# Kernel optimization log

Measured on AMD Instinct MI355X. Metric: run time of the kernel, lower is better.

The kernel has to match this reference:

```python
import jax, jax.numpy as jnp
import numpy as np
import math

# dims
B, S, HID = 1, 4096, 2048
NH = 16            # num_attention_heads
Q_LORA = 768
KV_LORA = 512
D_ROPE = 64        # qk_rope_head_dim
D_V = 128          # v_head_dim
TOP_K = 1024       # dsa_top_k
EPS = 1e-6
ROPE_BASE = 1e7
YARN_SCALE = 32.0


def _rms_norm(x, w, eps=EPS):
    xf = x.astype(jnp.float32)
    var = jnp.mean(xf * xf, axis=-1, keepdims=True)
    return (w * (xf * jax.lax.rsqrt(var + eps))).astype(x.dtype)


def _rotate_half(x):
    h = x.shape[-1] // 2
    return jnp.concatenate([-x[..., h:], x[..., :h]], axis=-1)


def _yarn_cos_sin(seq_len):
    # _yarn_find_correction_dims returns (mid, mid) => entire inv_freq is interpolated (divided by scale)
    inv_freq = 1.0 / (ROPE_BASE ** (jnp.arange(0, D_ROPE, 2, dtype=jnp.float32) / D_ROPE))
    inv_freq = inv_freq / YARN_SCALE
    t = jnp.arange(seq_len, dtype=jnp.float32) / YARN_SCALE
    freqs = t[:, None] * inv_freq[None, :]          # [S, D_ROPE/2]
    emb = jnp.concatenate([freqs, freqs], axis=-1)  # [S, D_ROPE]
    mscale2 = (0.1 * math.log(YARN_SCALE) + 1.0) ** 2  # mscale * mscale_all_dim
    return jnp.cos(emb) * mscale2, jnp.sin(emb) * mscale2


def setup_inputs() -> dict:
    key = jax.random.key(0)
    ks = jax.random.split(key, 10)
    std = 0.02
    return {
        'hidden_states': jax.random.normal(ks[0], (B, S, HID), dtype=jnp.float32),
        'position_ids': jnp.broadcast_to(jnp.arange(S), (B, S)),
        'dsa_indices': jnp.sort(jax.random.randint(ks[1], (B, 1, TOP_K), 0, S), axis=-1),
        'wq_a': jax.random.normal(ks[2], (HID, Q_LORA), dtype=jnp.float32) * std,
        'q_a_ln_w': jnp.ones((Q_LORA,), dtype=jnp.float32),
        'wq_b': jax.random.normal(ks[3], (Q_LORA, NH * D_V), dtype=jnp.float32) * std,
        'wq_rope': jax.random.normal(ks[4], (Q_LORA, NH * D_ROPE), dtype=jnp.float32) * std,
        'wkv_a': jax.random.normal(ks[5], (HID, KV_LORA + D_ROPE), dtype=jnp.float32) * std,
        'kv_a_ln_w': jnp.ones((KV_LORA,), dtype=jnp.float32),
        'wkv_b': jax.random.normal(ks[6], (KV_LORA, NH * 2 * D_V), dtype=jnp.float32) * std,
        'wo': jax.random.normal(ks[7], (NH * D_V, HID), dtype=jnp.float32) * std,
    }


def reference(hidden_states, position_ids, dsa_indices, wq_a, q_a_ln_w, wq_b,
              wq_rope, wkv_a, kv_a_ln_w, wkv_b, wo):
    bsz, seq_len, _ = hidden_states.shape

    # low-rank Q path (MLA)
    q_latent = _rms_norm(hidden_states @ wq_a, q_a_ln_w)            # [B,S,Q_LORA]
    q = (q_latent @ wq_b).reshape(bsz, seq_len, NH, D_V)            # [B,S,H,D_V]
    q_rope = (q_latent @ wq_rope).reshape(bsz, seq_len, NH, D_ROPE)

    # low-rank KV path with MQA rope channel
    kv_lr = hidden_states @ wkv_a                                   # [B,S,KV_LORA+D_ROPE]
    kv_latent = _rms_norm(kv_lr[..., :KV_LORA], kv_a_ln_w)
    k_rope = kv_lr[..., KV_LORA:]                                   # [B,S,D_ROPE]
    k_and_v = (kv_latent @ wkv_b).reshape(bsz, seq_len, NH, 2 * D_V)
    k = k_and_v[..., :D_V]
    v = k_and_v[..., D_V:]
    k_rope = jnp.broadcast_to(k_rope[:, :, None, :], (bsz, seq_len, NH, D_ROPE))

    # YaRN rotary embedding
    cos, sin = _yarn_cos_sin(seq_len)                               # [S,D_ROPE]
    cos_p = cos[position_ids][:, :, None, :]                        # [B,S,1,D_ROPE]
    sin_p = sin[position_ids][:, :, None, :]
    q_rope = q_rope * cos_p + _rotate_half(q_rope) * sin_p
    k_rope = k_rope * cos_p + _rotate_half(k_rope) * sin_p

    q_full = jnp.concatenate([q, q_rope], axis=-1)                  # [B,S,H,D_V+D_ROPE]
    k_full = jnp.concatenate([k, k_rope], axis=-1)

    # DSA: gather top-k KV positions per batch (dsa_indices[b,0,:])
    idx = dsa_indices[:, 0, :]                                      # [B,TOP_K]
    k_g = jnp.take_along_axis(k_full, idx[:, :, None, None], axis=1)  # [B,K,H,D]
    v_g = jnp.take_along_axis(v, idx[:, :, None, None], axis=1)       # [B,K,H,D_V]

    scale = 1.0 / math.sqrt(D_V + D_ROPE)
    scores = jnp.einsum('bqhd,bkhd->bhqk', q_full, k_g) * scale     # [B,H,S,K]
    probs = jax.nn.softmax(scores, axis=-1)
    attn = jnp.einsum('bhqk,bkhd->bqhd', probs, v_g)                # [B,S,H,D_V]
    out = attn.reshape(bsz, seq_len, NH * D_V) @ wo                 # [B,S,HID]
    return out
```

## Files before the change

kernel.cpp:

```cpp
#include <hip/hip_runtime.h>
#include <hip/hip_bf16.h>
#include <math.h>

#define S_LEN 4096
#define HIDDEN 2048
#define NH 16
#define QLORA 768
#define KVLORA 512
#define DROPE 64
#define DV 128
#define TOPK 1024
#define DQK 192

typedef __attribute__((ext_vector_type(4))) float f32x4;
typedef __attribute__((ext_vector_type(8))) __bf16 bf16x8;
typedef __attribute__((ext_vector_type(8))) unsigned short ushort8;
typedef unsigned short u16;
typedef unsigned int u32;

__device__ __forceinline__ u16 f2bf(float f) {
    union { float f; u32 u; } v; v.f = f;
    u32 r = v.u + 0x7fffu + ((v.u >> 16) & 1u);
    return (u16)(r >> 16);
}

__global__ __launch_bounds__(256) void k_cast(const float* __restrict__ src,
                                              u16* __restrict__ dst, int n4) {
    int i = blockIdx.x * 256 + threadIdx.x;
    if (i >= n4) return;
    float4 v = ((const float4*)src)[i];
    union { u16 h[4]; uint2 u; } o;
    o.h[0] = f2bf(v.x); o.h[1] = f2bf(v.y);
    o.h[2] = f2bf(v.z); o.h[3] = f2bf(v.w);
    ((uint2*)dst)[i] = o.u;
}

__global__ __launch_bounds__(256) void k_yarn(const int* __restrict__ pos_ids,
                                              float* __restrict__ cos_t,
                                              float* __restrict__ sin_t) {
    int idx = blockIdx.x * 256 + threadIdx.x;
    if (idx >= S_LEN * 32) return;
    int s = idx >> 5, i = idx & 31;
    float pos = (float)pos_ids[s];
    float inv = expf(-(float)i * 0.503690489092448f) * (1.0f / 1024.0f);
    float ang = pos * inv;
    const float MS2 = 1.8132604f;
    float sv, cv;
    sincosf(ang, &sv, &cv);
    cos_t[idx] = cv * MS2;
    sin_t[idx] = sv * MS2;
}

__global__ __launch_bounds__(256) void k_transpose(const float* __restrict__ src,
                                                   u16* __restrict__ dst,
                                                   int K, int N) {
    __shared__ u16 t[32][33];
    int n0 = blockIdx.x * 32, k0 = blockIdx.y * 32;
    int tx = threadIdx.x & 31, ty = threadIdx.x >> 5;
    #pragma unroll
    for (int i = 0; i < 32; i += 8)
        t[ty + i][tx] = f2bf(src[(long)(k0 + ty + i) * N + n0 + tx]);
    __syncthreads();
    #pragma unroll
    for (int i = 0; i < 32; i += 8)
        dst[(long)(n0 + ty + i) * K + k0 + tx] = t[tx][ty + i];
}

template <int MODE>
__global__ __launch_bounds__(256) void k_gemm(const u16* __restrict__ A,
                                              const u16* __restrict__ Bt,
                                              void* __restrict__ out0,
                                              void* __restrict__ out1,
                                              int M, int N, int K) {
    __shared__ u16 lA[128 * 40];
    __shared__ u16 lB[128 * 40];
    const int bm = blockIdx.y, bn = blockIdx.x;
    const int tid = threadIdx.x;
    const int lane = tid & 63, wid = tid >> 6;
    const int wr = wid >> 1, wc = wid & 1;
    const int l15 = lane & 15, l4 = lane >> 4;

    f32x4 acc[4][4];
    #pragma unroll
    for (int i = 0; i < 4; ++i)
        #pragma unroll
        for (int j = 0; j < 4; ++j) acc[i][j] = f32x4{0.f, 0.f, 0.f, 0.f};

    const int r = tid >> 1;
    const int ko = (tid & 1) * 16;
    const long arow = (long)bm * 128 + r;
    const int bcol = bn * 128 + r;
    const u16* pA = A + arow * K + ko;
    const u16* pB = Bt + (long)bcol * K + ko;
    const bool bok = (bcol < N);

    const int nkt = K >> 5;
    for (int kt = 0; kt < nkt; ++kt) {
        uint4 a0 = *(const uint4*)(pA);
        uint4 a1 = *(const uint4*)(pA + 8);
        uint4 b0 = bok ? *(const uint4*)(pB) : uint4{0, 0, 0, 0};
        uint4 b1 = bok ? *(const uint4*)(pB + 8) : uint4{0, 0, 0, 0};
        pA += 32; pB += 32;
        *(uint4*)(&lA[r * 40 + ko]) = a0;
        *(uint4*)(&lA[r * 40 + ko + 8]) = a1;
        *(uint4*)(&lB[r * 40 + ko]) = b0;
        *(uint4*)(&lB[r * 40 + ko + 8]) = b1;
        __syncthreads();

        bf16x8 af[4], bfr[4];
        #pragma unroll
        for (int mr = 0; mr < 4; ++mr)
            af[mr] = *(const bf16x8*)(&lA[(wr * 64 + mr * 16 + l15) * 40 + l4 * 8]);
        #pragma unroll
        for (int nc = 0; nc < 4; ++nc)
            bfr[nc] = *(const bf16x8*)(&lB[(wc * 64 + nc * 16 + l15) * 40 + l4 * 8]);
        #pragma unroll
        for (int mr = 0; mr < 4; ++mr)
            #pragma unroll
            for (int nc = 0; nc < 4; ++nc)
                acc[mr][nc] = __builtin_amdgcn_mfma_f32_16x16x32_bf16(
                    af[mr], bfr[nc], acc[mr][nc], 0, 0, 0);
        __syncthreads();
    }

    const int row0 = bm * 128 + wr * 64;
    const int col0 = bn * 128 + wc * 64;
    #pragma unroll
    for (int mr = 0; mr < 4; ++mr) {
        #pragma unroll
        for (int nc = 0; nc < 4; ++nc) {
            #pragma unroll
            for (int jj = 0; jj < 4; ++jj) {
                int row = row0 + mr * 16 + l4 * 4 + jj;
                int col = col0 + nc * 16 + l15;
                if (col >= N) continue;
                float v = acc[mr][nc][jj];
                if (MODE == 0) {
                    if (col < QLORA)
                        ((float*)out0)[(long)row * QLORA + col] = v;
                    else
                        ((float*)out1)[(long)row * (KVLORA + DROPE) + (col - QLORA)] = v;
                } else if (MODE == 1) {
                    if (col < NH * DV) {
                        int h = col >> 7, d = col & 127;
                        ((u16*)out0)[((long)h * S_LEN + row) * DQK + d] = f2bf(v);
                    } else {
                        int c2 = col - NH * DV;
                        ((u16*)out1)[(long)row * (NH * DROPE) + c2] = f2bf(v);
                    }
                } else if (MODE == 2) {
                    int h = col >> 8, rr = col & 255;
                    if (rr < 128)
                        ((u16*)out0)[((long)h * S_LEN + row) * DV + rr] = f2bf(v);
                    else
                        ((u16*)out1)[((long)h * S_LEN + row) * DV + (rr - 128)] = f2bf(v);
                } else {
                    ((float*)out0)[(long)row * N + col] = v;
                }
            }
        }
    }
}

__global__ __launch_bounds__(256) void k_rms_q(const float* __restrict__ q_lr,
                                               const float* __restrict__ w,
                                               u16* __restrict__ q_latent) {
    int s = blockIdx.x;
    const float* x = q_lr + (long)s * QLORA;
    int t = threadIdx.x;
    float v0 = x[t], v1 = x[t + 256], v2 = x[t + 512];
    float ss = v0 * v0 + v1 * v1 + v2 * v2;
    #pragma unroll
    for (int off = 32; off >= 1; off >>= 1) ss += __shfl_xor(ss, off);
    __shared__ float red[4];
    if ((t & 63) == 0) red[t >> 6] = ss;
    __syncthreads();
    ss = red[0] + red[1] + red[2] + red[3];
    float inv = rsqrtf(ss / (float)QLORA + 1e-6f);
    u16* o = q_latent + (long)s * QLORA;
    o[t]       = f2bf(v0 * inv * w[t]);
    o[t + 256] = f2bf(v1 * inv * w[t + 256]);
    o[t + 512] = f2bf(v2 * inv * w[t + 512]);
}

__global__ __launch_bounds__(256) void k_kv_norm_rope(const float* __restrict__ kv_lr,
                                                      const float* __restrict__ w,
                                                      const float* __restrict__ cos_t,
                                                      const float* __restrict__ sin_t,
                                                      u16* __restrict__ kv_latent,
                                                      u16* __restrict__ krope) {
    int s = blockIdx.x;
    const float* x = kv_lr + (long)s * (KVLORA + DROPE);
    int t = threadIdx.x;
    float v0 = x[t], v1 = x[t + 256];
    float ss = v0 * v0 + v1 * v1;
    #pragma unroll
    for (int off = 32; off >= 1; off >>= 1) ss += __shfl_xor(ss, off);
    __shared__ float red[4];
    if ((t & 63) == 0) red[t >> 6] = ss;
    __syncthreads();
    ss = red[0] + red[1] + red[2] + red[3];
    float inv = rsqrtf(ss / (float)KVLORA + 1e-6f);
    u16* o = kv_latent + (long)s * KVLORA;
    o[t]       = f2bf(v0 * inv * w[t]);
    o[t + 256] = f2bf(v1 * inv * w[t + 256]);
    if (t < DROPE) {
        int i = t & 31;
        float c = cos_t[s * 32 + i], sn = sin_t[s * 32 + i];
        float xr = x[KVLORA + t];
        float xp = x[KVLORA + ((t < 32) ? t + 32 : t - 32)];
        float val = (t < 32) ? xr * c - xp * sn : xr * c + xp * sn;
        krope[(long)s * DROPE + t] = f2bf(val);
    }
}

__global__ __launch_bounds__(256) void k_rope_q(const u16* __restrict__ q_rope_raw,
                                                const float* __restrict__ cos_t,
                                                const float* __restrict__ sin_t,
                                                u16* __restrict__ q_full) {
    long idx = (long)blockIdx.x * 256 + threadIdx.x;
    int s = (int)(idx >> 10);
    int rem = (int)(idx & 1023);
    int h = rem >> 6, j = rem & 63;
    int i = j & 31;
    float c = cos_t[s * 32 + i], sn = sin_t[s * 32 + i];
    const u16* base = q_rope_raw + (long)s * (NH * DROPE) + h * DROPE;
    union { u32 u; float f; } xr, xp;
    xr.u = ((u32)base[j]) << 16;
    xp.u = ((u32)base[(j < 32) ? j + 32 : j - 32]) << 16;
    float val = (j < 32) ? xr.f * c - xp.f * sn : xr.f * c + xp.f * sn;
    q_full[((long)h * S_LEN + s) * DQK + DV + j] = f2bf(val);
}

__global__ void k_gather(const int* __restrict__ idx,
                         const u16* __restrict__ k_buf,
                         const u16* __restrict__ v_buf,
                         const u16* __restrict__ krope,
                         u16* __restrict__ k_g, u16* __restrict__ v_g) {
    int j = blockIdx.x, h = blockIdx.y, t = threadIdx.x;
    int src = idx[j];
    const uint4* kb = (const uint4*)(k_buf + ((long)h * S_LEN + src) * DV);
    const uint4* vb = (const uint4*)(v_buf + ((long)h * S_LEN + src) * DV);
    const uint4* kr = (const uint4*)(krope + (long)src * DROPE);
    uint4* kgp = (uint4*)(k_g + ((long)h * TOPK + j) * DQK);
    uint4* vgp = (uint4*)(v_g + ((long)h * TOPK + j) * DV);
    if (t < 16)       kgp[t] = kb[t];
    else if (t < 24)  kgp[t] = kr[t - 16];
    else if (t < 40)  vgp[t - 24] = vb[t - 24];
}

__global__ __launch_bounds__(256) void k_attn(const u16* __restrict__ qf,
                                              const u16* __restrict__ kg,
                                              const u16* __restrict__ vg,
                                              u16* __restrict__ attn_out) {
    __shared__ u16 lK[64 * 200];
    __shared__ u16 lV[128 * 72];
    __shared__ u16 lP[4 * 16 * 72];
    const int h = blockIdx.y, qt = blockIdx.x;
    const int tid = threadIdx.x, lane = tid & 63, wid = tid >> 6;
    const int l15 = lane & 15, l4 = lane >> 4;

    bf16x8 qfr[6];
    {
        const u16* qrow = qf + ((long)h * S_LEN + qt * 64 + wid * 16 + l15) * DQK + l4 * 8;
        #pragma unroll
        for (int kd = 0; kd < 6; ++kd) qfr[kd] = *(const bf16x8*)(qrow + kd * 32);
    }
    float m[4] = {-1e30f, -1e30f, -1e30f, -1e30f};
    float l[4] = {0.f, 0.f, 0.f, 0.f};
    f32x4 acc_o[8];
    #pragma unroll
    for (int nc = 0; nc < 8; ++nc) acc_o[nc] = f32x4{0.f, 0.f, 0.f, 0.f};

    const int krow = tid >> 2, kseg = (tid & 3) * 48;
    const int vkey = tid >> 2, vseg = (tid & 3) * 32;
    const float scale = 0.07216878364870323f;

    for (int kt = 0; kt < TOPK / 64; ++kt) {
        {
            const u16* src = kg + ((long)h * TOPK + kt * 64 + krow) * DQK + kseg;
            u16* dst = &lK[krow * 200 + kseg];
            #pragma unroll
            for (int u = 0; u < 6; ++u)
                *(uint4*)(dst + u * 8) = *(const uint4*)(src + u * 8);
        }
        {
            const u16* src = vg + ((long)h * TOPK + kt * 64 + vkey) * DV + vseg;
            ushort8 dv[4];
            #pragma unroll
            for (int u = 0; u < 4; ++u) dv[u] = *(const ushort8*)(src + u * 8);
            #pragma unroll
            for (int u = 0; u < 4; ++u)
                #pragma unroll
                for (int e = 0; e < 8; ++e)
                    lV[(vseg + u * 8 + e) * 72 + vkey] = dv[u][e];
        }
        __syncthreads();

        f32x4 sa[4];
        #pragma unroll
        for (int kc = 0; kc < 4; ++kc) {
            sa[kc] = f32x4{0.f, 0.f, 0.f, 0.f};
            #pragma unroll
            for (int kd = 0; kd < 6; ++kd) {
                bf16x8 kf = *(const bf16x8*)(&lK[(kc * 16 + l15) * 200 + kd * 32 + l4 * 8]);
                sa[kc] = __builtin_amdgcn_mfma_f32_16x16x32_bf16(qfr[kd], kf, sa[kc], 0, 0, 0);
            }
            sa[kc] *= scale;
        }
        float fac[4], psum[4];
        #pragma unroll
        for (int jj = 0; jj < 4; ++jj) {
            float mx = fmaxf(fmaxf(sa[0][jj], sa[1][jj]), fmaxf(sa[2][jj], sa[3][jj]));
            #pragma unroll
            for (int off = 1; off <= 8; off <<= 1) mx = fmaxf(mx, __shfl_xor(mx, off));
            float mnew = fmaxf(m[jj], mx);
            fac[jj] = __expf(m[jj] - mnew);
            m[jj] = mnew;
            psum[jj] = 0.f;
        }
        #pragma unroll
        for (int kc = 0; kc < 4; ++kc) {
            #pragma unroll
            for (int jj = 0; jj < 4; ++jj) {
                float p = __expf(sa[kc][jj] - m[jj]);
                psum[jj] += p;
                lP[(wid * 16 + l4 * 4 + jj) * 72 + kc * 16 + l15] = f2bf(p);
            }
        }
        #pragma unroll
        for (int jj = 0; jj < 4; ++jj) {
            #pragma unroll
            for (int off = 1; off <= 8; off <<= 1) psum[jj] += __shfl_xor(psum[jj], off);
            l[jj] = l[jj] * fac[jj] + psum[jj];
        }
        #pragma unroll
        for (int nc = 0; nc < 8; ++nc)
            #pragma unroll
            for (int jj = 0; jj < 4; ++jj) acc_o[nc][jj] *= fac[jj];
        #pragma unroll
        for (int kc2 = 0; kc2 < 2; ++kc2) {
            bf16x8 pf = *(const bf16x8*)(&lP[(wid * 16 + l15) * 72 + kc2 * 32 + l4 * 8]);
            #pragma unroll
            for (int nc = 0; nc < 8; ++nc) {
                bf16x8 vf = *(const bf16x8*)(&lV[(nc * 16 + l15) * 72 + kc2 * 32 + l4 * 8]);
                acc_o[nc] = __builtin_amdgcn_mfma_f32_16x16x32_bf16(pf, vf, acc_o[nc], 0, 0, 0);
            }
        }
        __syncthreads();
    }
    int row = qt * 64 + wid * 16 + l4 * 4;
    #pragma unroll
    for (int nc = 0; nc < 8; ++nc)
        #pragma unroll
        for (int jj = 0; jj < 4; ++jj) {
            float v = acc_o[nc][jj] / l[jj];
            attn_out[(long)(row + jj) * (NH * DV) + h * DV + nc * 16 + l15] = f2bf(v);
        }
}

extern "C" void kernel_launch(void* const* d_in, const int* in_sizes, int n_in,
                              void* d_out, int out_size, void* d_ws, size_t ws_size,
                              hipStream_t stream) {
    const float* hs      = (const float*)d_in[0];
    const int*   pos     = (const int*)d_in[1];
    const int*   dsa     = (const int*)d_in[2];
    const float* wq_a    = (const float*)d_in[3];
    const float* q_ln    = (const float*)d_in[4];
    const float* wq_b    = (const float*)d_in[5];
    const float* wq_rope = (const float*)d_in[6];
    const float* wkv_a   = (const float*)d_in[7];
    const float* kv_ln   = (const float*)d_in[8];
    const float* wkv_b   = (const float*)d_in[9];
    const float* wo      = (const float*)d_in[10];
    float* out = (float*)d_out;

    char* ws = (char*)d_ws;
    auto alloc = [&](size_t bytes) {
        char* p = ws; ws += (bytes + 255) & ~(size_t)255; return p;
    };
    u16* W1t  = (u16*)alloc(1344L * 2048 * 2);
    u16* W2t  = (u16*)alloc(3072L * 768 * 2);
    u16* W3t  = (u16*)alloc(4096L * 512 * 2);
    u16* W4t  = (u16*)alloc(2048L * 2048 * 2);
    float* q_lr  = (float*)alloc(4096L * 768 * 4);
    float* kv_lr = (float*)alloc(4096L * 576 * 4);
    u16* q_latent   = (u16*)alloc(4096L * 768 * 2);
    u16* kv_latent  = (u16*)alloc(4096L * 512 * 2);
    u16* q_rope_raw = (u16*)alloc(4096L * 1024 * 2);
    u16* q_full     = (u16*)alloc(16L * 4096 * 192 * 2);
    u16* k_buf      = (u16*)alloc(16L * 4096 * 128 * 2);
    u16* v_buf      = (u16*)alloc(16L * 4096 * 128 * 2);
    float* cos_t    = (float*)alloc(4096L * 32 * 4);
    float* sin_t    = (float*)alloc(4096L * 32 * 4);
    char* late = alloc(16L * 4096 * 2 * 2 > (16L * 1024 * 192 + 16L * 1024 * 128 + 4096L * 64) * 2
                       ? 16L * 4096 * 2 * 2
                       : (16L * 1024 * 192 + 16L * 1024 * 128 + 4096L * 64) * 2);
    u16* hs_bf = (u16*)late;
    u16* k_g   = (u16*)late;
    u16* v_g   = k_g + 16L * 1024 * 192;
    u16* krope = v_g + 16L * 1024 * 128;
    u16* attn_o = (u16*)q_lr;

    k_yarn<<<dim3(512), dim3(256), 0, stream>>>(pos, cos_t, sin_t);
    k_cast<<<dim3(8192), dim3(256), 0, stream>>>(hs, hs_bf, 4096 * 2048 / 4);

    k_transpose<<<dim3(768 / 32, 2048 / 32), 256, 0, stream>>>(wq_a, W1t, 2048, 768);
    k_transpose<<<dim3(576 / 32, 2048 / 32), 256, 0, stream>>>(wkv_a, W1t + 768L * 2048, 2048, 576);
    k_transpose<<<dim3(2048 / 32, 768 / 32), 256, 0, stream>>>(wq_b, W2t, 768, 2048);
    k_transpose<<<dim3(1024 / 32, 768 / 32), 256, 0, stream>>>(wq_rope, W2t + 2048L * 768, 768, 1024);
    k_transpose<<<dim3(4096 / 32, 512 / 32), 256, 0, stream>>>(wkv_b, W3t, 512, 4096);
    k_transpose<<<dim3(2048 / 32, 2048 / 32), 256, 0, stream>>>(wo, W4t, 2048, 2048);

    k_gemm<0><<<dim3(11, 32), 256, 0, stream>>>(hs_bf, W1t, q_lr, kv_lr, 4096, 1344, 2048);
    k_rms_q<<<4096, 256, 0, stream>>>(q_lr, q_ln, q_latent);
    k_kv_norm_rope<<<4096, 256, 0, stream>>>(kv_lr, kv_ln, cos_t, sin_t, kv_latent, krope);
    k_gemm<1><<<dim3(24, 32), 256, 0, stream>>>(q_latent, W2t, q_full, q_rope_raw, 4096, 3072, 768);
    k_rope_q<<<16384, 256, 0, stream>>>(q_rope_raw, cos_t, sin_t, q_full);
    k_gemm<2><<<dim3(32, 32), 256, 0, stream>>>(kv_latent, W3t, k_buf, v_buf, 4096, 4096, 512);
    k_gather<<<dim3(1024, 16), 64, 0, stream>>>(dsa, k_buf, v_buf, krope, k_g, v_g);
    k_attn<<<dim3(64, 16), 256, 0, stream>>>(q_full, k_g, v_g, attn_o);
    k_gemm<3><<<dim3(16, 32), 256, 0, stream>>>(attn_o, W4t, out, nullptr, 4096, 2048, 2048);
}
```

Baseline: 513.7 us.

## Use direct global-to-LDS loads in GEMM, fuse q RoPE, pre-transpose V, widen attention tiles

The GEMM now stages A and B tiles with global_load_lds (16-byte async copies straight into unpadded LDS) instead of register round-trips, and pads W1t to 1408 columns so the N bound check can go. Query RoPE is fused into the MODE 1 GEMM epilogue, which removes the separate rope kernel and the q_rope_raw buffer. The gather kernel writes V pre-transposed per 64-key tile so attention can copy it into LDS with vector stores, and attention now handles 128 queries per block with a remapped head/tile order. Risks: the unpadded LDS may cause bank conflicts, the padded W1t rows are never written (their outputs are discarded), and the attention block holds more registers.

Result: faster. 502.4 us (-2.2%).

```diff
diff --git a/kernel.cpp b/kernel.cpp
--- a/kernel.cpp
+++ b/kernel.cpp
@@ -14,7 +14,6 @@
 
 typedef __attribute__((ext_vector_type(4))) float f32x4;
 typedef __attribute__((ext_vector_type(8))) __bf16 bf16x8;
-typedef __attribute__((ext_vector_type(8))) unsigned short ushort8;
 typedef unsigned short u16;
 typedef unsigned int u32;
 
@@ -22,6 +21,10 @@
     union { float f; u32 u; } v; v.f = f;
     u32 r = v.u + 0x7fffu + ((v.u >> 16) & 1u);
     return (u16)(r >> 16);
+}
+
+__device__ __forceinline__ void gll16(const u16* g, u16* l) {
+    __builtin_amdgcn_global_load_lds((const void*)g, (void*)l, 16, 0, 0);
 }
 
 __global__ __launch_bounds__(256) void k_cast(const float* __restrict__ src,
@@ -71,9 +74,11 @@
                                               const u16* __restrict__ Bt,
                                               void* __restrict__ out0,
                                               void* __restrict__ out1,
+                                              const float* __restrict__ cos_t,
+                                              const float* __restrict__ sin_t,
                                               int M, int N, int K) {
-    __shared__ u16 lA[128 * 40];
-    __shared__ u16 lB[128 * 40];
+    __shared__ u16 lA[128 * 32];
+    __shared__ u16 lB[128 * 32];
     const int bm = blockIdx.y, bn = blockIdx.x;
     const int tid = threadIdx.x;
     const int lane = tid & 63, wid = tid >> 6;
@@ -86,34 +91,31 @@
         #pragma unroll
         for (int j = 0; j < 4; ++j) acc[i][j] = f32x4{0.f, 0.f, 0.f, 0.f};
 
-    const int r = tid >> 1;
-    const int ko = (tid & 1) * 16;
-    const long arow = (long)bm * 128 + r;
-    const int bcol = bn * 128 + r;
-    const u16* pA = A + arow * K + ko;
-    const u16* pB = Bt + (long)bcol * K + ko;
-    const bool bok = (bcol < N);
+    const int srow = wid * 32 + (lane >> 2);
+    const int scol = (lane & 3) * 8;
+    const u16* gA = A + (long)(bm * 128 + srow) * K + scol;
+    const u16* gB = Bt + (long)(bn * 128 + srow) * K + scol;
+    u16* lA0 = lA + wid * 1024;
+    u16* lB0 = lB + wid * 1024;
+    const long kstep16 = 16L * K;
 
     const int nkt = K >> 5;
     for (int kt = 0; kt < nkt; ++kt) {
-        uint4 a0 = *(const uint4*)(pA);
-        uint4 a1 = *(const uint4*)(pA + 8);
-        uint4 b0 = bok ? *(const uint4*)(pB) : uint4{0, 0, 0, 0};
-        uint4 b1 = bok ? *(const uint4*)(pB + 8) : uint4{0, 0, 0, 0};
-        pA += 32; pB += 32;
-        *(uint4*)(&lA[r * 40 + ko]) = a0;
-        *(uint4*)(&lA[r * 40 + ko + 8]) = a1;
-        *(uint4*)(&lB[r * 40 + ko]) = b0;
-        *(uint4*)(&lB[r * 40 + ko + 8]) = b1;
+        const u16* pa = gA + kt * 32;
+        const u16* pb = gB + kt * 32;
+        gll16(pa, lA0);
+        gll16(pa + kstep16, lA0 + 512);
+        gll16(pb, lB0);
+        gll16(pb + kstep16, lB0 + 512);
         __syncthreads();
 
         bf16x8 af[4], bfr[4];
         #pragma unroll
         for (int mr = 0; mr < 4; ++mr)
-            af[mr] = *(const bf16x8*)(&lA[(wr * 64 + mr * 16 + l15) * 40 + l4 * 8]);
+            af[mr] = *(const bf16x8*)(&lA[(wr * 64 + mr * 16 + l15) * 32 + l4 * 8]);
         #pragma unroll
         for (int nc = 0; nc < 4; ++nc)
-            bfr[nc] = *(const bf16x8*)(&lB[(wc * 64 + nc * 16 + l15) * 40 + l4 * 8]);
+            bfr[nc] = *(const bf16x8*)(&lB[(wc * 64 + nc * 16 + l15) * 32 + l4 * 8]);
         #pragma unroll
         for (int mr = 0; mr < 4; ++mr)
             #pragma unroll
@@ -133,12 +135,11 @@
             for (int jj = 0; jj < 4; ++jj) {
                 int row = row0 + mr * 16 + l4 * 4 + jj;
                 int col = col0 + nc * 16 + l15;
-                if (col >= N) continue;
                 float v = acc[mr][nc][jj];
                 if (MODE == 0) {
                     if (col < QLORA)
                         ((float*)out0)[(long)row * QLORA + col] = v;
-                    else
+                    else if (col < QLORA + KVLORA + DROPE)
                         ((float*)out1)[(long)row * (KVLORA + DROPE) + (col - QLORA)] = v;
                 } else if (MODE == 1) {
                     if (col < NH * DV) {
@@ -146,7 +147,11 @@
                         ((u16*)out0)[((long)h * S_LEN + row) * DQK + d] = f2bf(v);
                     } else {
                         int c2 = col - NH * DV;
-                        ((u16*)out1)[(long)row * (NH * DROPE) + c2] = f2bf(v);
+                        int h = c2 >> 6, j = c2 & 63, i = j & 31;
+                        float c = cos_t[row * 32 + i], sn = sin_t[row * 32 + i];
+                        float xp = acc[mr][nc ^ 2][jj];
+                        float val = (j < 32) ? v * c - xp * sn : v * c + xp * sn;
+                        ((u16*)out0)[((long)h * S_LEN + row) * DQK + DV + j] = f2bf(val);
                     }
                 } else if (MODE == 2) {
                     int h = col >> 8, rr = col & 255;
@@ -214,66 +219,58 @@
     }
 }
 
-__global__ __launch_bounds__(256) void k_rope_q(const u16* __restrict__ q_rope_raw,
-                                                const float* __restrict__ cos_t,
-                                                const float* __restrict__ sin_t,
-                                                u16* __restrict__ q_full) {
-    long idx = (long)blockIdx.x * 256 + threadIdx.x;
-    int s = (int)(idx >> 10);
-    int rem = (int)(idx & 1023);
-    int h = rem >> 6, j = rem & 63;
-    int i = j & 31;
-    float c = cos_t[s * 32 + i], sn = sin_t[s * 32 + i];
-    const u16* base = q_rope_raw + (long)s * (NH * DROPE) + h * DROPE;
-    union { u32 u; float f; } xr, xp;
-    xr.u = ((u32)base[j]) << 16;
-    xp.u = ((u32)base[(j < 32) ? j + 32 : j - 32]) << 16;
-    float val = (j < 32) ? xr.f * c - xp.f * sn : xr.f * c + xp.f * sn;
-    q_full[((long)h * S_LEN + s) * DQK + DV + j] = f2bf(val);
-}
-
 __global__ void k_gather(const int* __restrict__ idx,
                          const u16* __restrict__ k_buf,
                          const u16* __restrict__ v_buf,
                          const u16* __restrict__ krope,
-                         u16* __restrict__ k_g, u16* __restrict__ v_g) {
+                         u16* __restrict__ k_g, u16* __restrict__ v_g_t) {
     int j = blockIdx.x, h = blockIdx.y, t = threadIdx.x;
     int src = idx[j];
     const uint4* kb = (const uint4*)(k_buf + ((long)h * S_LEN + src) * DV);
-    const uint4* vb = (const uint4*)(v_buf + ((long)h * S_LEN + src) * DV);
     const uint4* kr = (const uint4*)(krope + (long)src * DROPE);
     uint4* kgp = (uint4*)(k_g + ((long)h * TOPK + j) * DQK);
-    uint4* vgp = (uint4*)(v_g + ((long)h * TOPK + j) * DV);
     if (t < 16)       kgp[t] = kb[t];
     else if (t < 24)  kgp[t] = kr[t - 16];
-    else if (t < 40)  vgp[t - 24] = vb[t - 24];
+    u32 vv = *(const u32*)(v_buf + ((long)h * S_LEN + src) * DV + t * 2);
+    int kt = j >> 6, jin = j & 63;
+    u16* base = v_g_t + ((long)(h * 16 + kt) * 128) * 64 + jin;
+    base[(2 * t) * 64]     = (u16)(vv & 0xffff);
+    base[(2 * t + 1) * 64] = (u16)(vv >> 16);
 }
 
 __global__ __launch_bounds__(256) void k_attn(const u16* __restrict__ qf,
                                               const u16* __restrict__ kg,
-                                              const u16* __restrict__ vg,
+                                              const u16* __restrict__ vgt,
                                               u16* __restrict__ attn_out) {
     __shared__ u16 lK[64 * 200];
-    __shared__ u16 lV[128 * 72];
-    __shared__ u16 lP[4 * 16 * 72];
-    const int h = blockIdx.y, qt = blockIdx.x;
+    __shared__ u16 lVt[128 * 72];
+    __shared__ u16 lP[4][16 * 72];
+    const int b = blockIdx.x;
+    const int h = (b & 7) * 2 + ((b >> 3) & 1);
+    const int qt = b >> 4;
     const int tid = threadIdx.x, lane = tid & 63, wid = tid >> 6;
     const int l15 = lane & 15, l4 = lane >> 4;
 
-    bf16x8 qfr[6];
-    {
-        const u16* qrow = qf + ((long)h * S_LEN + qt * 64 + wid * 16 + l15) * DQK + l4 * 8;
-        #pragma unroll
-        for (int kd = 0; kd < 6; ++kd) qfr[kd] = *(const bf16x8*)(qrow + kd * 32);
-    }
-    float m[4] = {-1e30f, -1e30f, -1e30f, -1e30f};
-    float l[4] = {0.f, 0.f, 0.f, 0.f};
-    f32x4 acc_o[8];
-    #pragma unroll
-    for (int nc = 0; nc < 8; ++nc) acc_o[nc] = f32x4{0.f, 0.f, 0.f, 0.f};
+    bf16x8 qfr[2][6];
+    #pragma unroll
+    for (int qs = 0; qs < 2; ++qs) {
+        const u16* qrow = qf + ((long)h * S_LEN + qt * 128 + wid * 32 + qs * 16 + l15) * DQK + l4 * 8;
+        #pragma unroll
+        for (int kd = 0; kd < 6; ++kd) qfr[qs][kd] = *(const bf16x8*)(qrow + kd * 32);
+    }
+    float m[2][4], l[2][4];
+    #pragma unroll
+    for (int qs = 0; qs < 2; ++qs)
+        #pragma unroll
+        for (int jj = 0; jj < 4; ++jj) { m[qs][jj] = -1e30f; l[qs][jj] = 0.f; }
+    f32x4 acc_o[2][8];
+    #pragma unroll
+    for (int qs = 0; qs < 2; ++qs)
+        #pragma unroll
+        for (int nc = 0; nc < 8; ++nc) acc_o[qs][nc] = f32x4{0.f, 0.f, 0.f, 0.f};
 
     const int krow = tid >> 2, kseg = (tid & 3) * 48;
-    const int vkey = tid >> 2, vseg = (tid & 3) * 32;
+    u16* lPw = lP[wid];
     const float scale = 0.07216878364870323f;
 
     for (int kt = 0; kt < TOPK / 64; ++kt) {
@@ -285,78 +282,80 @@
                 *(uint4*)(dst + u * 8) = *(const uint4*)(src + u * 8);
         }
         {
-            const u16* src = vg + ((long)h * TOPK + kt * 64 + vkey) * DV + vseg;
-            ushort8 dv[4];
-            #pragma unroll
-            for (int u = 0; u < 4; ++u) dv[u] = *(const ushort8*)(src + u * 8);
-            #pragma unroll
-            for (int u = 0; u < 4; ++u)
-                #pragma unroll
-                for (int e = 0; e < 8; ++e)
-                    lV[(vseg + u * 8 + e) * 72 + vkey] = dv[u][e];
+            const u16* src = vgt + ((long)(h * 16 + kt) * 128) * 64 + tid * 32;
+            u16* dst = &lVt[(tid >> 1) * 72 + (tid & 1) * 32];
+            #pragma unroll
+            for (int c = 0; c < 4; ++c)
+                *(uint4*)(dst + c * 8) = *(const uint4*)(src + c * 8);
         }
         __syncthreads();
 
-        f32x4 sa[4];
-        #pragma unroll
-        for (int kc = 0; kc < 4; ++kc) {
-            sa[kc] = f32x4{0.f, 0.f, 0.f, 0.f};
-            #pragma unroll
-            for (int kd = 0; kd < 6; ++kd) {
-                bf16x8 kf = *(const bf16x8*)(&lK[(kc * 16 + l15) * 200 + kd * 32 + l4 * 8]);
-                sa[kc] = __builtin_amdgcn_mfma_f32_16x16x32_bf16(qfr[kd], kf, sa[kc], 0, 0, 0);
-            }
-            sa[kc] *= scale;
-        }
-        float fac[4], psum[4];
-        #pragma unroll
-        for (int jj = 0; jj < 4; ++jj) {
-            float mx = fmaxf(fmaxf(sa[0][jj], sa[1][jj]), fmaxf(sa[2][jj], sa[3][jj]));
-            #pragma unroll
-            for (int off = 1; off <= 8; off <<= 1) mx = fmaxf(mx, __shfl_xor(mx, off));
-            float mnew = fmaxf(m[jj], mx);
-            fac[jj] = __expf(m[jj] - mnew);
-            m[jj] = mnew;
-            psum[jj] = 0.f;
-        }
-        #pragma unroll
-        for (int kc = 0; kc < 4; ++kc) {
+        #pragma unroll
+        for (int qs = 0; qs < 2; ++qs) {
+            f32x4 sa[4];
+            #pragma unroll
+            for (int kc = 0; kc < 4; ++kc) {
+                sa[kc] = f32x4{0.f, 0.f, 0.f, 0.f};
+                #pragma unroll
+                for (int kd = 0; kd < 6; ++kd) {
+                    bf16x8 kf = *(const bf16x8*)(&lK[(kc * 16 + l15) * 200 + kd * 32 + l4 * 8]);
+                    sa[kc] = __builtin_amdgcn_mfma_f32_16x16x32_bf16(qfr[qs][kd], kf, sa[kc], 0, 0, 0);
+                }
+                sa[kc] *= scale;
+            }
+            float fac[4], psum[4];
             #pragma unroll
             for (int jj = 0; jj < 4; ++jj) {
-                float p = __expf(sa[kc][jj] - m[jj]);
-                psum[jj] += p;
-                lP[(wid * 16 + l4 * 4 + jj) * 72 + kc * 16 + l15] = f2bf(p);
-            }
-        }
-        #pragma unroll
-        for (int jj = 0; jj < 4; ++jj) {
-            #pragma unroll
-            for (int off = 1; off <= 8; off <<= 1) psum[jj] += __shfl_xor(psum[jj], off);
-            l[jj] = l[jj] * fac[jj] + psum[jj];
-        }
-        #pragma unroll
-        for (int nc = 0; nc < 8; ++nc)
-            #pragma unroll
-            for (int jj = 0; jj < 4; ++jj) acc_o[nc][jj] *= fac[jj];
-        #pragma unroll
-        for (int kc2 = 0; kc2 < 2; ++kc2) {
-            bf16x8 pf = *(const bf16x8*)(&lP[(wid * 16 + l15) * 72 + kc2 * 32 + l4 * 8]);
-            #pragma unroll
-            for (int nc = 0; nc < 8; ++nc) {
-                bf16x8 vf = *(const bf16x8*)(&lV[(nc * 16 + l15) * 72 + kc2 * 32 + l4 * 8]);
-                acc_o[nc] = __builtin_amdgcn_mfma_f32_16x16x32_bf16(pf, vf, acc_o[nc], 0, 0, 0);
+                float mx = fmaxf(fmaxf(sa[0][jj], sa[1][jj]), fmaxf(sa[2][jj], sa[3][jj]));
+                #pragma unroll
+                for (int off = 1; off <= 8; off <<= 1) mx = fmaxf(mx, __shfl_xor(mx, off));
+                float mnew = fmaxf(m[qs][jj], mx);
+                fac[jj] = __expf(m[qs][jj] - mnew);
+                m[qs][jj] = mnew;
+                psum[jj] = 0.f;
+            }
+            #pragma unroll
+            for (int kc = 0; kc < 4; ++kc) {
+                #pragma unroll
+                for (int jj = 0; jj < 4; ++jj) {
+                    float p = __expf(sa[kc][jj] - m[qs][jj]);
+                    psum[jj] += p;
+                    lPw[(l4 * 4 + jj) * 72 + kc * 16 + l15] = f2bf(p);
+                }
+            }
+            #pragma unroll
+            for (int jj = 0; jj < 4; ++jj) {
+                #pragma unroll
+                for (int off = 1; off <= 8; off <<= 1) psum[jj] += __shfl_xor(psum[jj], off);
+                l[qs][jj] = l[qs][jj] * fac[jj] + psum[jj];
+            }
+            #pragma unroll
+            for (int nc = 0; nc < 8; ++nc)
+                #pragma unroll
+                for (int jj = 0; jj < 4; ++jj) acc_o[qs][nc][jj] *= fac[jj];
+            #pragma unroll
+            for (int kc2 = 0; kc2 < 2; ++kc2) {
+                bf16x8 pf = *(const bf16x8*)(&lPw[l15 * 72 + kc2 * 32 + l4 * 8]);
+                #pragma unroll
+                for (int nc = 0; nc < 8; ++nc) {
+                    bf16x8 vf = *(const bf16x8*)(&lVt[(nc * 16 + l15) * 72 + kc2 * 32 + l4 * 8]);
+                    acc_o[qs][nc] = __builtin_amdgcn_mfma_f32_16x16x32_bf16(pf, vf, acc_o[qs][nc], 0, 0, 0);
+                }
             }
         }
         __syncthreads();
     }
-    int row = qt * 64 + wid * 16 + l4 * 4;
-    #pragma unroll
-    for (int nc = 0; nc < 8; ++nc)
-        #pragma unroll
-        for (int jj = 0; jj < 4; ++jj) {
-            float v = acc_o[nc][jj] / l[jj];
-            attn_out[(long)(row + jj) * (NH * DV) + h * DV + nc * 16 + l15] = f2bf(v);
-        }
+    #pragma unroll
+    for (int qs = 0; qs < 2; ++qs) {
+        int row = qt * 128 + wid * 32 + qs * 16 + l4 * 4;
+        #pragma unroll
+        for (int nc = 0; nc < 8; ++nc)
+            #pragma unroll
+            for (int jj = 0; jj < 4; ++jj) {
+                float v = acc_o[qs][nc][jj] / l[qs][jj];
+                attn_out[(long)(row + jj) * (NH * DV) + h * DV + nc * 16 + l15] = f2bf(v);
+            }
+    }
 }
 
 extern "C" void kernel_launch(void* const* d_in, const int* in_sizes, int n_in,
@@ -379,7 +378,7 @@
     auto alloc = [&](size_t bytes) {
         char* p = ws; ws += (bytes + 255) & ~(size_t)255; return p;
     };
-    u16* W1t  = (u16*)alloc(1344L * 2048 * 2);
+    u16* W1t  = (u16*)alloc(1408L * 2048 * 2);
     u16* W2t  = (u16*)alloc(3072L * 768 * 2);
     u16* W3t  = (u16*)alloc(4096L * 512 * 2);
     u16* W4t  = (u16*)alloc(2048L * 2048 * 2);
@@ -387,19 +386,16 @@
     float* kv_lr = (float*)alloc(4096L * 576 * 4);
     u16* q_latent   = (u16*)alloc(4096L * 768 * 2);
     u16* kv_latent  = (u16*)alloc(4096L * 512 * 2);
-    u16* q_rope_raw = (u16*)alloc(4096L * 1024 * 2);
     u16* q_full     = (u16*)alloc(16L * 4096 * 192 * 2);
     u16* k_buf      = (u16*)alloc(16L * 4096 * 128 * 2);
     u16* v_buf      = (u16*)alloc(16L * 4096 * 128 * 2);
     float* cos_t    = (float*)alloc(4096L * 32 * 4);
     float* sin_t    = (float*)alloc(4096L * 32 * 4);
-    char* late = alloc(16L * 4096 * 2 * 2 > (16L * 1024 * 192 + 16L * 1024 * 128 + 4096L * 64) * 2
-                       ? 16L * 4096 * 2 * 2
-                       : (16L * 1024 * 192 + 16L * 1024 * 128 + 4096L * 64) * 2);
+    char* late = alloc(16L * 4096 * 2 * 2);
     u16* hs_bf = (u16*)late;
     u16* k_g   = (u16*)late;
-    u16* v_g   = k_g + 16L * 1024 * 192;
-    u16* krope = v_g + 16L * 1024 * 128;
+    u16* v_g_t = k_g + 16L * 1024 * 192;
+    u16* krope = v_g_t + 16L * 1024 * 128;
     u16* attn_o = (u16*)q_lr;
 
     k_yarn<<<dim3(512), dim3(256), 0, stream>>>(pos, cos_t, sin_t);
@@ -412,13 +408,12 @@
     k_transpose<<<dim3(4096 / 32, 512 / 32), 256, 0, stream>>>(wkv_b, W3t, 512, 4096);
     k_transpose<<<dim3(2048 / 32, 2048 / 32), 256, 0, stream>>>(wo, W4t, 2048, 2048);
 
-    k_gemm<0><<<dim3(11, 32), 256, 0, stream>>>(hs_bf, W1t, q_lr, kv_lr, 4096, 1344, 2048);
+    k_gemm<0><<<dim3(11, 32), 256, 0, stream>>>(hs_bf, W1t, q_lr, kv_lr, nullptr, nullptr, 4096, 1408, 2048);
     k_rms_q<<<4096, 256, 0, stream>>>(q_lr, q_ln, q_latent);
     k_kv_norm_rope<<<4096, 256, 0, stream>>>(kv_lr, kv_ln, cos_t, sin_t, kv_latent, krope);
-    k_gemm<1><<<dim3(24, 32), 256, 0, stream>>>(q_latent, W2t, q_full, q_rope_raw, 4096, 3072, 768);
-    k_rope_q<<<16384, 256, 0, stream>>>(q_rope_raw, cos_t, sin_t, q_full);
-    k_gemm<2><<<dim3(32, 32), 256, 0, stream>>>(kv_latent, W3t, k_buf, v_buf, 4096, 4096, 512);
-    k_gather<<<dim3(1024, 16), 64, 0, stream>>>(dsa, k_buf, v_buf, krope, k_g, v_g);
-    k_attn<<<dim3(64, 16), 256, 0, stream>>>(q_full, k_g, v_g, attn_o);
-    k_gemm<3><<<dim3(16, 32), 256, 0, stream>>>(attn_o, W4t, out, nullptr, 4096, 2048, 2048);
-}
+    k_gemm<1><<<dim3(24, 32), 256, 0, stream>>>(q_latent, W2t, q_full, nullptr, cos_t, sin_t, 4096, 3072, 768);
+    k_gemm<2><<<dim3(32, 32), 256, 0, stream>>>(kv_latent, W3t, k_buf, v_buf, nullptr, nullptr, 4096, 4096, 512);
+    k_gather<<<dim3(1024, 16), 64, 0, stream>>>(dsa, k_buf, v_buf, krope, k_g, v_g_t);
+    k_attn<<<dim3(512), 256, 0, stream>>>(q_full, k_g, v_g_t, attn_o);
+    k_gemm<3><<<dim3(16, 32), 256, 0, stream>>>(attn_o, W4t, out, nullptr, nullptr, nullptr, 4096, 2048, 2048);
+}
```
